# Kernel optimization log

Measured on AMD Instinct MI355X. Metric: run time of the kernel, lower is better.

Reference implementation:

```python
import jax, jax.numpy as jnp
import numpy as np

B, T, C, H = 256, 256, 64, 512


def _uni(key, shape, stdv):
    return jax.random.uniform(key, shape, minval=-stdv, maxval=stdv, dtype=jnp.float32)


def setup_inputs() -> dict:
    key = jax.random.key(0)
    ks = jax.random.split(key, 16)
    data = jax.random.normal(ks[0], (B, T, C), dtype=jnp.float32)
    nan_mask = jax.random.uniform(ks[1], (B, T, C)) < 0.2
    data = jnp.where(nan_mask, jnp.nan, data)
    s_lstm = 1.0 / np.sqrt(H)
    s_c = 1.0 / np.sqrt(C)
    s_h = 1.0 / np.sqrt(H)
    return {
        'data': data,
        # LSTMCell (input = 2*C), PyTorch gate order i,f,g,o
        'W_ih': _uni(ks[2], (4 * H, 2 * C), s_lstm),
        'W_hh': _uni(ks[3], (4 * H, H), s_lstm),
        'b_ih': _uni(ks[4], (4 * H,), s_lstm),
        'b_hh': _uni(ks[5], (4 * H,), s_lstm),
        # temp_decay_h: TemporalDecay(C -> H), stdv = 1/sqrt(W.size(0)) = 1/sqrt(H)
        'W_gh': _uni(ks[6], (H, C), s_h),
        'b_gh': _uni(ks[7], (H,), s_h),
        # temp_decay_x: diag TemporalDecay(C -> C)
        'W_gx': _uni(ks[8], (C, C), s_c),
        'b_gx': _uni(ks[9], (C,), s_c),
        # hist_reg: Linear(H -> C)
        'W_hist': _uni(ks[10], (C, H), s_h),
        'b_hist': _uni(ks[11], (C,), s_h),
        'W_feat': _uni(ks[12], (C, C), s_c),
        'b_feat': _uni(ks[13], (C,), s_c),
        # weight_combine: Linear(2C -> C)
        'W_comb': _uni(ks[14], (C, 2 * C), 1.0 / np.sqrt(2 * C)),
        'b_comb': _uni(ks[15], (C,), 1.0 / np.sqrt(2 * C)),
    }


def delta_calc(masks):
    # masks: [B, T, C]. delta[:,0]=0; delta[:,1]=1; for t>=2:
    # decay = 1 if mask[:,t-1]==1 else decay+1, delta[:,t]=decay.
    b, t, c = masks.shape
    m_prev = jnp.moveaxis(masks[:, 1:t - 1, :], 1, 0)  # [T-2, B, C]

    def step(decay, mp):
        nd = jnp.where(mp == 1.0, 1.0, decay + 1.0)
        return nd, nd

    _, ds = jax.lax.scan(step, jnp.ones((b, c), masks.dtype), m_prev)
    return jnp.concatenate(
        [jnp.zeros((b, 1, c), masks.dtype),
         jnp.ones((b, 1, c), masks.dtype),
         jnp.moveaxis(ds, 0, 1)], axis=1)


def reference(data, W_ih, W_hh, b_ih, b_hh, W_gh, b_gh, W_gx, b_gx,
              W_hist, b_hist, W_feat, b_feat, W_comb, b_comb):
    masks = (~jnp.isnan(data)).astype(data.dtype)
    values = jnp.nan_to_num(data)
    deltas = delta_calc(masks)
    c_dim = data.shape[-1]
    eye = jnp.eye(c_dim, dtype=data.dtype)
    W_gx_m = W_gx * eye            # diag TemporalDecay mask
    W_feat_m = W_feat * (1.0 - eye)

    xs = (jnp.moveaxis(values, 1, 0), jnp.moveaxis(masks, 1, 0),
          jnp.moveaxis(deltas, 1, 0))  # time-major [T,B,C]

    def step(carry, tmd):
        h, c = carry
        x, m, d = tmd
        gamma_h = jnp.exp(-jax.nn.relu(d @ W_gh.T + b_gh))
        gamma_x = jnp.exp(-jax.nn.relu(d @ W_gx_m.T + b_gx))
        h = h * gamma_h
        x_h = h @ W_hist.T + b_hist
        x_c = m * x + (1.0 - m) * x_h
        z_h = x_c @ W_feat_m.T + b_feat
        alpha = jnp.concatenate([gamma_x, m], axis=1) @ W_comb.T + b_comb
        c_h = alpha * z_h + (1.0 - alpha) * x_h
        c_c = m * x + (1.0 - m) * c_h
        inp = jnp.concatenate([c_c, m], axis=1)
        gates = inp @ W_ih.T + b_ih + h @ W_hh.T + b_hh
        gi, gf, gg, go = jnp.split(gates, 4, axis=1)
        c_new = jax.nn.sigmoid(gf) * c + jax.nn.sigmoid(gi) * jnp.tanh(gg)
        h_new = jax.nn.sigmoid(go) * jnp.tanh(c_new)
        return (h_new, c_new), c_c

    hb = data.shape[0]
    hd = W_hh.shape[1]
    init = (jnp.zeros((hb, hd), data.dtype), jnp.zeros((hb, hd), data.dtype))
    _, imps = jax.lax.scan(step, init, xs)
    return jnp.moveaxis(imps, 0, 1)  # [B, T, C]
```

## Files before the change

kernel.cpp:

```cpp
#include <hip/hip_runtime.h>

typedef unsigned short ushort_t;
typedef unsigned int uint_t;
typedef unsigned long long ull_t;
typedef short v8s __attribute__((ext_vector_type(8)));
typedef float v4f __attribute__((ext_vector_type(4)));

__device__ __forceinline__ float b2f(ushort_t u) {
    uint_t x = ((uint_t)u) << 16;
    float f;
    __builtin_memcpy(&f, &x, 4);
    return f;
}
__device__ __forceinline__ ushort_t f2b(float f) {
    uint_t x;
    __builtin_memcpy(&x, &f, 4);
    uint_t r = (x + 0x7FFFu + ((x >> 16) & 1u)) >> 16;
    return (ushort_t)r;
}

__global__ __launch_bounds__(256) void k_setup(
    const float* __restrict__ Wih, const float* __restrict__ Whh,
    const float* __restrict__ Wgh, const float* __restrict__ Whist,
    const float* __restrict__ Wfeat,
    ushort_t* __restrict__ Wih_b, ushort_t* __restrict__ Whh_b,
    ushort_t* __restrict__ Wgh_b, ushort_t* __restrict__ Whist_b,
    ushort_t* __restrict__ Wfeat_b, ull_t* __restrict__ hbufs) {
    int bid = blockIdx.x, tid = threadIdx.x;
    if (bid < 64) {
        ull_t* p = hbufs + (size_t)bid * 4096 + tid;
#pragma unroll
        for (int i = 0; i < 16; ++i) p[i * 256] = 0;
        return;
    }
    bid -= 64;
    const float* src; ushort_t* dst; int n;
    if (bid < 1024)      { src = Wih;   dst = Wih_b;   n = 262144; }
    else if (bid < 5120) { bid -= 1024; src = Whh;   dst = Whh_b;   n = 1048576; }
    else if (bid < 5248) { bid -= 5120; src = Wgh;   dst = Wgh_b;   n = 32768; }
    else if (bid < 5376) { bid -= 5248; src = Whist; dst = Whist_b; n = 32768; }
    else                 { bid -= 5376; src = Wfeat; dst = Wfeat_b; n = 4096; }
    int i = bid * 256 + tid;
    if (i < n) dst[i] = f2b(src[i]);
}

__global__ __launch_bounds__(256) void k_pre(
    const float* __restrict__ data, const float* __restrict__ Wgx,
    const float* __restrict__ bgx,
    ushort_t* __restrict__ values, ushort_t* __restrict__ masks,
    ushort_t* __restrict__ deltas, ushort_t* __restrict__ gammax) {
    __shared__ int lastl[32][9];
    int tid = threadIdx.x;
    int j = tid >> 5, p = tid & 31;
    int pid = blockIdx.x * 32 + p;
    int b = pid >> 6, c = pid & 63;
    float wd = Wgx[c * 64 + c], bg = bgx[c];
    int t0 = j * 32;
    const float* dp = data + (size_t)b * 16384 + c;
    float v[32]; uint_t bits = 0;
#pragma unroll
    for (int s = 0; s < 32; ++s) {
        float x = dp[(t0 + s) * 64];
        bool obs = (x == x);
        v[s] = obs ? x : 0.f;
        bits |= obs ? (1u << s) : 0u;
    }
    uint_t vb = bits;
    if (j == 0) vb &= ~1u;
    int lastloc = 0;
    if (vb) lastloc = t0 + (31 - __clz(vb));
    lastl[p][j] = lastloc;
    __syncthreads();
    int L = 0;
    for (int jj = 0; jj < j; ++jj) L = max(L, lastl[p][jj]);
#pragma unroll
    for (int s = 0; s < 32; ++s) {
        int t = t0 + s;
        float m = ((bits >> s) & 1) ? 1.f : 0.f;
        float d = (t == 0) ? 0.f : (float)(t - L);
        float sg = d * wd + bg;
        float gx = (sg > 0.f) ? __expf(-sg) : 1.f;
        size_t o = (size_t)t * 16384 + pid;
        values[o] = f2b(v[s]); masks[o] = f2b(m);
        deltas[o] = f2b(d);    gammax[o] = f2b(gx);
        if (((bits >> s) & 1) && t >= 1) L = t;
    }
}

__global__ __launch_bounds__(256) void k_alpha(
    const ushort_t* __restrict__ gammax, const ushort_t* __restrict__ masks,
    const float* __restrict__ Wcomb, const float* __restrict__ bcomb,
    ushort_t* __restrict__ alpha) {
    __shared__ __attribute__((aligned(16))) ushort_t wl[64 * 136];
    __shared__ __attribute__((aligned(16))) ushort_t al[16 * 136];
    int tid = threadIdx.x;
    for (int idx = tid; idx < 8192; idx += 256) {
        int r = idx >> 7, kcol = idx & 127;
        wl[r * 136 + kcol] = f2b(Wcomb[idx]);
    }
    int tb0 = blockIdx.x * 16;
    for (int idx = tid; idx < 2048; idx += 256) {
        int r = idx >> 7, kcol = idx & 127;
        al[r * 136 + kcol] = (kcol < 64)
            ? gammax[(size_t)(tb0 + r) * 64 + kcol]
            : masks[(size_t)(tb0 + r) * 64 + (kcol - 64)];
    }
    __syncthreads();
    int i = tid & 63, rg = (tid >> 6) * 4;
    float bc = bcomb[i];
    float acc[4] = {bc, bc, bc, bc};
#pragma unroll
    for (int k8 = 0; k8 < 16; ++k8) {
        v8s w8 = *(const v8s*)(wl + i * 136 + k8 * 8);
#pragma unroll
        for (int rr = 0; rr < 4; ++rr) {
            v8s a8 = *(const v8s*)(al + (rg + rr) * 136 + k8 * 8);
#pragma unroll
            for (int q = 0; q < 8; ++q)
                acc[rr] += b2f((ushort_t)a8[q]) * b2f((ushort_t)w8[q]);
        }
    }
#pragma unroll
    for (int rr = 0; rr < 4; ++rr)
        alpha[(size_t)(tb0 + rg + rr) * 64 + i] = f2b(acc[rr]);
}

__global__ __launch_bounds__(256, 1) void k_run(
    const ushort_t* __restrict__ values, const ushort_t* __restrict__ masks,
    const ushort_t* __restrict__ deltas, const ushort_t* __restrict__ alpha,
    const ushort_t* __restrict__ Wih, const ushort_t* __restrict__ Whh,
    const float* __restrict__ bih, const float* __restrict__ bhh,
    const ushort_t* __restrict__ Wgh, const float* __restrict__ bgh,
    const ushort_t* __restrict__ Whist, const float* __restrict__ bhist,
    const ushort_t* __restrict__ Wfeat, const float* __restrict__ bfeat,
    ushort_t* __restrict__ hbufs, float* __restrict__ out) {
    __shared__ __attribute__((aligned(16))) ushort_t hlds[16 * 520];
    __shared__ __attribute__((aligned(16))) ushort_t inplds[16 * 136];
    __shared__ __attribute__((aligned(16))) ushort_t xclds[16 * 72];
    __shared__ __attribute__((aligned(16))) ushort_t d1b[16 * 72];
    __shared__ __attribute__((aligned(16))) float gl[4 * 16 * 36];
    __shared__ __attribute__((aligned(16))) float gam[16 * 36];

    int tid = threadIdx.x;
    int w = tid >> 6;
    int lane = tid & 63;
    int l15 = lane & 15, quad = lane >> 4;
    int wg = blockIdx.x;
    int rb = wg & 15, cb = wg >> 4;
    int b0 = rb * 16;

    v8s whhF[2][16], wihF[2][4], whisF[16], wfF[2], wghF[2] = {};
    float biasv[2];
#pragma unroll
    for (int nt2 = 0; nt2 < 2; ++nt2) {
        int hc = cb * 32 + nt2 * 16 + l15;
        int rW = w * 512 + hc;
        const ushort_t* whrow = Whh + (size_t)rW * 512;
        const ushort_t* wirow = Wih + (size_t)rW * 128;
#pragma unroll
        for (int kt = 0; kt < 16; ++kt)
            whhF[nt2][kt] = *(const v8s*)(whrow + kt * 32 + quad * 8);
#pragma unroll
        for (int kt = 0; kt < 4; ++kt)
            wihF[nt2][kt] = *(const v8s*)(wirow + kt * 32 + quad * 8);
        biasv[nt2] = bih[rW] + bhh[rW];
    }
    int colC = w * 16 + l15;
    {
        const ushort_t* hrow = Whist + (size_t)colC * 512;
#pragma unroll
        for (int kt = 0; kt < 16; ++kt)
            whisF[kt] = *(const v8s*)(hrow + kt * 32 + quad * 8);
        const ushort_t* frow = Wfeat + colC * 64;
#pragma unroll
        for (int kt = 0; kt < 2; ++kt) {
            int k0 = kt * 32 + quad * 8;
            v8s bb = *(const v8s*)(frow + k0);
#pragma unroll
            for (int j = 0; j < 8; ++j)
                if (k0 + j == colC) bb[j] = 0;
            wfF[kt] = bb;
        }
    }
    float bghv = 0.f;
    if (w < 2) {
        int gcol = cb * 32 + w * 16 + l15;
        const ushort_t* grow = Wgh + gcol * 64;
#pragma unroll
        for (int kt = 0; kt < 2; ++kt)
            wghF[kt] = *(const v8s*)(grow + kt * 32 + quad * 8);
        bghv = bgh[gcol];
    }
    float bhistv = bhist[colC];
    float bfeatv = bfeat[colC];

    int sf_row = tid >> 3, sf_c4 = (tid & 7) * 4;
    float c_reg4[4] = {0.f, 0.f, 0.f, 0.f};

    for (int t = 0; t < 256; ++t) {
        float v4r[4], m4r[4], a4r[4];
#pragma unroll
        for (int r = 0; r < 4; ++r) {
            int row = quad * 4 + r;
            size_t g = (size_t)t * 16384 + (b0 + row) * 64 + colC;
            v4r[r] = b2f(values[g]);
            m4r[r] = b2f(masks[g]);
            a4r[r] = b2f(alpha[g]);
        }
        v8s mreg = {}, dreg = {};
        if (tid < 128) {
            int row = tid >> 3, c8 = (tid & 7) * 8;
            int tn = (t < 255) ? t + 1 : 255;
            mreg = *(const v8s*)(masks + (size_t)t * 16384 + (b0 + row) * 64 + c8);
            dreg = *(const v8s*)(deltas + (size_t)tn * 16384 + (b0 + row) * 64 + c8);
        }

        if (t == 0) {
            v8s z = {0, 0, 0, 0, 0, 0, 0, 0};
            for (int idx = tid; idx < 1040; idx += 256) ((v8s*)hlds)[idx] = z;
        } else {
            const ushort_t* hb = hbufs + (size_t)(t & 7) * 131072;
            const ull_t* hp[8];
            ull_t hv[8];
#pragma unroll
            for (int i = 0; i < 8; ++i) {
                int c = tid + 256 * i;
                int row = c >> 7, c4 = (c & 127) * 4;
                hp[i] = (const ull_t*)(hb + (b0 + row) * 512 + c4);
                hv[i] = __hip_atomic_load(hp[i], __ATOMIC_RELAXED,
                                          __HIP_MEMORY_SCOPE_AGENT);
            }
            int guard = 0;
            while (true) {
                bool any = false;
#pragma unroll
                for (int i = 0; i < 8; ++i) any |= (hv[i] == 0);
                if (!any || ++guard > (1 << 20)) break;
                __builtin_amdgcn_s_sleep(1);
#pragma unroll
                for (int i = 0; i < 8; ++i)
                    if (hv[i] == 0)
                        hv[i] = __hip_atomic_load(hp[i], __ATOMIC_RELAXED,
                                                  __HIP_MEMORY_SCOPE_AGENT);
            }
#pragma unroll
            for (int i = 0; i < 8; ++i) {
                int c = tid + 256 * i;
                int row = c >> 7, c4 = (c & 127) * 4;
                *(ull_t*)(hlds + row * 520 + c4) =
                    hv[i] - 0x0001000100010001ULL;
            }
        }
        if (tid < 128) {
            int row = tid >> 3, c8 = (tid & 7) * 8;
            *(v8s*)(inplds + row * 136 + 64 + c8) = mreg;
            *(v8s*)(d1b + row * 72 + c8) = dreg;
        }
        __syncthreads();

        v4f accx = {0.f, 0.f, 0.f, 0.f};
        v4f accg0 = {0.f, 0.f, 0.f, 0.f}, accg1 = {0.f, 0.f, 0.f, 0.f};
#pragma unroll
        for (int kt = 0; kt < 16; ++kt) {
            v8s a = *(const v8s*)(hlds + l15 * 520 + kt * 32 + quad * 8);
            accx = __builtin_amdgcn_mfma_f32_16x16x32_bf16(a, whisF[kt], accx, 0, 0, 0);
            accg0 = __builtin_amdgcn_mfma_f32_16x16x32_bf16(a, whhF[0][kt], accg0, 0, 0, 0);
            accg1 = __builtin_amdgcn_mfma_f32_16x16x32_bf16(a, whhF[1][kt], accg1, 0, 0, 0);
        }
        if (w < 2) {
            v4f acc = {0.f, 0.f, 0.f, 0.f};
#pragma unroll
            for (int kt = 0; kt < 2; ++kt) {
                v8s a = *(const v8s*)(d1b + l15 * 72 + kt * 32 + quad * 8);
                acc = __builtin_amdgcn_mfma_f32_16x16x32_bf16(a, wghF[kt], acc, 0, 0, 0);
            }
#pragma unroll
            for (int r = 0; r < 4; ++r) {
                float s = acc[r] + bghv;
                gam[(quad * 4 + r) * 36 + w * 16 + l15] = (s > 0.f) ? __expf(-s) : 1.f;
            }
        }
        float xh4[4];
#pragma unroll
        for (int r = 0; r < 4; ++r) {
            float xh = accx[r] + bhistv;
            float xc = m4r[r] * v4r[r] + (1.f - m4r[r]) * xh;
            xclds[(quad * 4 + r) * 72 + colC] = f2b(xc);
            xh4[r] = xh;
        }
        __syncthreads();

        {
            v4f accz = {0.f, 0.f, 0.f, 0.f};
#pragma unroll
            for (int kt = 0; kt < 2; ++kt) {
                v8s a = *(const v8s*)(xclds + l15 * 72 + kt * 32 + quad * 8);
                accz = __builtin_amdgcn_mfma_f32_16x16x32_bf16(a, wfF[kt], accz, 0, 0, 0);
            }
#pragma unroll
            for (int r = 0; r < 4; ++r) {
                float zh = accz[r] + bfeatv;
                float ch = a4r[r] * zh + (1.f - a4r[r]) * xh4[r];
                float cc = m4r[r] * v4r[r] + (1.f - m4r[r]) * ch;
                int row = quad * 4 + r;
                inplds[row * 136 + colC] = f2b(cc);
                if (cb == 0)
                    out[(size_t)(b0 + row) * 16384 + t * 64 + colC] = cc;
            }
        }
        __syncthreads();

#pragma unroll
        for (int nt2 = 0; nt2 < 2; ++nt2) {
            v4f acc = (nt2 == 0) ? accg0 : accg1;
#pragma unroll
            for (int kt = 0; kt < 4; ++kt) {
                v8s a = *(const v8s*)(inplds + l15 * 136 + kt * 32 + quad * 8);
                acc = __builtin_amdgcn_mfma_f32_16x16x32_bf16(a, wihF[nt2][kt], acc, 0, 0, 0);
            }
#pragma unroll
            for (int r = 0; r < 4; ++r)
                gl[w * 576 + (quad * 4 + r) * 36 + nt2 * 16 + l15] = acc[r] + biasv[nt2];
        }
        __syncthreads();

        if (tid < 128) {
            ull_t outv = 0;
#pragma unroll
            for (int j = 0; j < 4; ++j) {
                int hcl = sf_c4 + j;
                float gi = gl[0 * 576 + sf_row * 36 + hcl];
                float gf = gl[1 * 576 + sf_row * 36 + hcl];
                float gg = gl[2 * 576 + sf_row * 36 + hcl];
                float go = gl[3 * 576 + sf_row * 36 + hcl];
                float si = 1.f / (1.f + __expf(-gi));
                float sf = 1.f / (1.f + __expf(-gf));
                float tg = 1.f - 2.f / (__expf(2.f * gg) + 1.f);
                float so = 1.f / (1.f + __expf(-go));
                float cn = sf * c_reg4[j] + si * tg;
                c_reg4[j] = cn;
                float hn = so * (1.f - 2.f / (__expf(2.f * cn) + 1.f));
                float g = gam[sf_row * 36 + hcl];
                outv |= (ull_t)(ushort_t)(f2b(hn * g) + 1) << (16 * j);
            }
            size_t myoff = (size_t)(b0 + sf_row) * 512 + cb * 32 + sf_c4;
            if (t < 255) {
                ushort_t* hnx = hbufs + (size_t)((t + 1) & 7) * 131072;
                __hip_atomic_store((ull_t*)(hnx + myoff), outv,
                                   __ATOMIC_RELAXED, __HIP_MEMORY_SCOPE_AGENT);
            }
            if (t + 4 < 256) {
                ushort_t* hz = hbufs + (size_t)((t + 4) & 7) * 131072;
                __hip_atomic_store((ull_t*)(hz + myoff), 0ULL,
                                   __ATOMIC_RELAXED, __HIP_MEMORY_SCOPE_AGENT);
            }
        }
        __syncthreads();
    }
}

extern "C" void kernel_launch(void* const* d_in, const int* in_sizes, int n_in,
                              void* d_out, int out_size, void* d_ws, size_t ws_size,
                              hipStream_t stream) {
    const float* data  = (const float*)d_in[0];
    const float* Wih   = (const float*)d_in[1];
    const float* Whh   = (const float*)d_in[2];
    const float* bih   = (const float*)d_in[3];
    const float* bhh   = (const float*)d_in[4];
    const float* Wgh   = (const float*)d_in[5];
    const float* bgh   = (const float*)d_in[6];
    const float* Wgx   = (const float*)d_in[7];
    const float* bgx   = (const float*)d_in[8];
    const float* Whist = (const float*)d_in[9];
    const float* bhist = (const float*)d_in[10];
    const float* Wfeat = (const float*)d_in[11];
    const float* bfeat = (const float*)d_in[12];
    const float* Wcomb = (const float*)d_in[13];
    const float* bcomb = (const float*)d_in[14];
    float* out = (float*)d_out;

    char* ws = (char*)d_ws;
    const size_t NTBC = 256UL * 256 * 64;
    ushort_t* valuesb = (ushort_t*)ws; ws += NTBC * 2;
    ushort_t* masksp  = (ushort_t*)ws; ws += NTBC * 2;
    ushort_t* deltasp = (ushort_t*)ws; ws += NTBC * 2;
    ushort_t* gammax  = (ushort_t*)ws; ws += NTBC * 2;
    ushort_t* alphap  = (ushort_t*)ws; ws += NTBC * 2;
    ushort_t* Wih_b   = (ushort_t*)ws; ws += 2048UL * 128 * 2;
    ushort_t* Whh_b   = (ushort_t*)ws; ws += 2048UL * 512 * 2;
    ushort_t* Wgh_b   = (ushort_t*)ws; ws += 512UL * 64 * 2;
    ushort_t* Whist_b = (ushort_t*)ws; ws += 64UL * 512 * 2;
    ushort_t* Wfeat_b = (ushort_t*)ws; ws += 64UL * 64 * 2;
    ushort_t* hbufs   = (ushort_t*)ws; ws += 8UL * 131072 * 2;

    k_setup<<<5456, 256, 0, stream>>>(Wih, Whh, Wgh, Whist, Wfeat,
                                      Wih_b, Whh_b, Wgh_b, Whist_b, Wfeat_b,
                                      (ull_t*)hbufs);
    k_pre<<<512, 256, 0, stream>>>(data, Wgx, bgx, valuesb, masksp, deltasp, gammax);
    k_alpha<<<4096, 256, 0, stream>>>(gammax, masksp, Wcomb, bcomb, alphap);
    k_run<<<256, 256, 0, stream>>>(valuesb, masksp, deltasp, alphap,
                                   Wih_b, Whh_b, bih, bhh,
                                   Wgh_b, bgh, Whist_b, bhist,
                                   Wfeat_b, bfeat, hbufs, out);
}
```

Baseline: 973.0 us.

## Prefetch next-step inputs, use MFMA in alpha kernel, lighter barriers, spread output writes

The recurrent kernel now loads the per-step values, masks, alpha and deltas for the next timestep while the current step runs, which takes global load latency off the serial path. Its __syncthreads calls become a custom barrier that waits only on LDS counters. Gate and gamma LDS rows are padded to 44 floats so they can be read as vectors, and poll addresses are computed once. Output writes rotate across column-blocks instead of always coming from cb==0. The alpha kernel is rewritten around bf16 MFMA with 64 rows per block. Risks are higher register pressure and relying on correct ordering with a weaker barrier.

```diff
diff --git a/kernel.cpp b/kernel.cpp
--- a/kernel.cpp
+++ b/kernel.cpp
@@ -17,6 +17,12 @@
     __builtin_memcpy(&x, &f, 4);
     uint_t r = (x + 0x7FFFu + ((x >> 16) & 1u)) >> 16;
     return (ushort_t)r;
+}
+
+__device__ __forceinline__ void wg_bar() {
+    asm volatile("s_waitcnt lgkmcnt(0)" ::: "memory");
+    __builtin_amdgcn_s_barrier();
+    asm volatile("" ::: "memory");
 }
 
 __global__ __launch_bounds__(256) void k_setup(
@@ -92,37 +98,41 @@
     const float* __restrict__ Wcomb, const float* __restrict__ bcomb,
     ushort_t* __restrict__ alpha) {
     __shared__ __attribute__((aligned(16))) ushort_t wl[64 * 136];
-    __shared__ __attribute__((aligned(16))) ushort_t al[16 * 136];
+    __shared__ __attribute__((aligned(16))) ushort_t al[64 * 136];
     int tid = threadIdx.x;
     for (int idx = tid; idx < 8192; idx += 256) {
         int r = idx >> 7, kcol = idx & 127;
         wl[r * 136 + kcol] = f2b(Wcomb[idx]);
     }
-    int tb0 = blockIdx.x * 16;
-    for (int idx = tid; idx < 2048; idx += 256) {
+    int tb0 = blockIdx.x * 64;
+    for (int idx = tid; idx < 8192; idx += 256) {
         int r = idx >> 7, kcol = idx & 127;
         al[r * 136 + kcol] = (kcol < 64)
             ? gammax[(size_t)(tb0 + r) * 64 + kcol]
             : masks[(size_t)(tb0 + r) * 64 + (kcol - 64)];
     }
     __syncthreads();
-    int i = tid & 63, rg = (tid >> 6) * 4;
-    float bc = bcomb[i];
-    float acc[4] = {bc, bc, bc, bc};
-#pragma unroll
-    for (int k8 = 0; k8 < 16; ++k8) {
-        v8s w8 = *(const v8s*)(wl + i * 136 + k8 * 8);
-#pragma unroll
-        for (int rr = 0; rr < 4; ++rr) {
-            v8s a8 = *(const v8s*)(al + (rg + rr) * 136 + k8 * 8);
-#pragma unroll
-            for (int q = 0; q < 8; ++q)
-                acc[rr] += b2f((ushort_t)a8[q]) * b2f((ushort_t)w8[q]);
-        }
-    }
-#pragma unroll
-    for (int rr = 0; rr < 4; ++rr)
-        alpha[(size_t)(tb0 + rg + rr) * 64 + i] = f2b(acc[rr]);
+    int w = tid >> 6, lane = tid & 63, l15 = lane & 15, quad = lane >> 4;
+    v4f acc[4] = {};
+#pragma unroll
+    for (int kt = 0; kt < 4; ++kt) {
+        v8s a = *(const v8s*)(al + (w * 16 + l15) * 136 + kt * 32 + quad * 8);
+#pragma unroll
+        for (int nt = 0; nt < 4; ++nt) {
+            v8s bfr = *(const v8s*)(wl + (nt * 16 + l15) * 136 + kt * 32 + quad * 8);
+            acc[nt] = __builtin_amdgcn_mfma_f32_16x16x32_bf16(a, bfr, acc[nt], 0, 0, 0);
+        }
+    }
+#pragma unroll
+    for (int nt = 0; nt < 4; ++nt) {
+        int col = nt * 16 + l15;
+        float bc = bcomb[col];
+#pragma unroll
+        for (int j = 0; j < 4; ++j) {
+            int row = w * 16 + quad * 4 + j;
+            alpha[(size_t)(tb0 + row) * 64 + col] = f2b(acc[nt][j] + bc);
+        }
+    }
 }
 
 __global__ __launch_bounds__(256, 1) void k_run(
@@ -138,8 +148,8 @@
     __shared__ __attribute__((aligned(16))) ushort_t inplds[16 * 136];
     __shared__ __attribute__((aligned(16))) ushort_t xclds[16 * 72];
     __shared__ __attribute__((aligned(16))) ushort_t d1b[16 * 72];
-    __shared__ __attribute__((aligned(16))) float gl[4 * 16 * 36];
-    __shared__ __attribute__((aligned(16))) float gam[16 * 36];
+    __shared__ __attribute__((aligned(16))) float gl[4 * 16 * 44];
+    __shared__ __attribute__((aligned(16))) float gam[16 * 44];
 
     int tid = threadIdx.x;
     int w = tid >> 6;
@@ -195,41 +205,46 @@
     float bfeatv = bfeat[colC];
 
     int sf_row = tid >> 3, sf_c4 = (tid & 7) * 4;
+    int srow = sf_row, sc8 = (tid & 7) * 8;
+
+    int pollQ[8], ldsB[8];
+#pragma unroll
+    for (int i = 0; i < 8; ++i) {
+        int c = tid + 256 * i;
+        int row = c >> 7, c4 = (c & 127) * 4;
+        pollQ[i] = ((b0 + row) * 512 + c4) >> 2;
+        ldsB[i] = row * 520 + c4;
+    }
+
+    ushort_t vraw[4], mraw[4], araw[4];
+    v8s mregc = {}, dregc = {};
+#pragma unroll
+    for (int r = 0; r < 4; ++r) {
+        size_t g = (size_t)(b0 + quad * 4 + r) * 64 + colC;
+        vraw[r] = values[g]; mraw[r] = masks[g]; araw[r] = alpha[g];
+    }
+    if (tid < 128) {
+        mregc = *(const v8s*)(masks + (size_t)(b0 + srow) * 64 + sc8);
+        dregc = *(const v8s*)(deltas + 16384 + (size_t)(b0 + srow) * 64 + sc8);
+    }
+
     float c_reg4[4] = {0.f, 0.f, 0.f, 0.f};
 
     for (int t = 0; t < 256; ++t) {
-        float v4r[4], m4r[4], a4r[4];
-#pragma unroll
-        for (int r = 0; r < 4; ++r) {
-            int row = quad * 4 + r;
-            size_t g = (size_t)t * 16384 + (b0 + row) * 64 + colC;
-            v4r[r] = b2f(values[g]);
-            m4r[r] = b2f(masks[g]);
-            a4r[r] = b2f(alpha[g]);
-        }
-        v8s mreg = {}, dreg = {};
         if (tid < 128) {
-            int row = tid >> 3, c8 = (tid & 7) * 8;
-            int tn = (t < 255) ? t + 1 : 255;
-            mreg = *(const v8s*)(masks + (size_t)t * 16384 + (b0 + row) * 64 + c8);
-            dreg = *(const v8s*)(deltas + (size_t)tn * 16384 + (b0 + row) * 64 + c8);
-        }
-
+            *(v8s*)(inplds + srow * 136 + 64 + sc8) = mregc;
+            *(v8s*)(d1b + srow * 72 + sc8) = dregc;
+        }
         if (t == 0) {
             v8s z = {0, 0, 0, 0, 0, 0, 0, 0};
             for (int idx = tid; idx < 1040; idx += 256) ((v8s*)hlds)[idx] = z;
         } else {
-            const ushort_t* hb = hbufs + (size_t)(t & 7) * 131072;
-            const ull_t* hp[8];
+            const ull_t* hq = (const ull_t*)(hbufs + (size_t)(t & 7) * 131072);
             ull_t hv[8];
 #pragma unroll
-            for (int i = 0; i < 8; ++i) {
-                int c = tid + 256 * i;
-                int row = c >> 7, c4 = (c & 127) * 4;
-                hp[i] = (const ull_t*)(hb + (b0 + row) * 512 + c4);
-                hv[i] = __hip_atomic_load(hp[i], __ATOMIC_RELAXED,
+            for (int i = 0; i < 8; ++i)
+                hv[i] = __hip_atomic_load(hq + pollQ[i], __ATOMIC_RELAXED,
                                           __HIP_MEMORY_SCOPE_AGENT);
-            }
             int guard = 0;
             while (true) {
                 bool any = false;
@@ -240,23 +255,31 @@
 #pragma unroll
                 for (int i = 0; i < 8; ++i)
                     if (hv[i] == 0)
-                        hv[i] = __hip_atomic_load(hp[i], __ATOMIC_RELAXED,
+                        hv[i] = __hip_atomic_load(hq + pollQ[i], __ATOMIC_RELAXED,
                                                   __HIP_MEMORY_SCOPE_AGENT);
             }
 #pragma unroll
-            for (int i = 0; i < 8; ++i) {
-                int c = tid + 256 * i;
-                int row = c >> 7, c4 = (c & 127) * 4;
-                *(ull_t*)(hlds + row * 520 + c4) =
-                    hv[i] - 0x0001000100010001ULL;
-            }
-        }
-        if (tid < 128) {
-            int row = tid >> 3, c8 = (tid & 7) * 8;
-            *(v8s*)(inplds + row * 136 + 64 + c8) = mreg;
-            *(v8s*)(d1b + row * 72 + c8) = dreg;
-        }
-        __syncthreads();
+            for (int i = 0; i < 8; ++i)
+                *(ull_t*)(hlds + ldsB[i]) = hv[i] - 0x0001000100010001ULL;
+        }
+        ushort_t vnx[4], mnx[4], anx[4];
+        v8s mregn = mregc, dregn = dregc;
+        {
+            int tp = (t < 255) ? t + 1 : 255;
+            int tq = (t < 254) ? t + 2 : 255;
+            size_t gb = (size_t)tp * 16384;
+#pragma unroll
+            for (int r = 0; r < 4; ++r) {
+                size_t g = gb + (size_t)(b0 + quad * 4 + r) * 64 + colC;
+                vnx[r] = values[g]; mnx[r] = masks[g]; anx[r] = alpha[g];
+            }
+            if (tid < 128) {
+                mregn = *(const v8s*)(masks + gb + (size_t)(b0 + srow) * 64 + sc8);
+                dregn = *(const v8s*)(deltas + (size_t)tq * 16384 +
+                                      (size_t)(b0 + srow) * 64 + sc8);
+            }
+        }
+        wg_bar();
 
         v4f accx = {0.f, 0.f, 0.f, 0.f};
         v4f accg0 = {0.f, 0.f, 0.f, 0.f}, accg1 = {0.f, 0.f, 0.f, 0.f};
@@ -277,10 +300,14 @@
 #pragma unroll
             for (int r = 0; r < 4; ++r) {
                 float s = acc[r] + bghv;
-                gam[(quad * 4 + r) * 36 + w * 16 + l15] = (s > 0.f) ? __expf(-s) : 1.f;
-            }
-        }
-        float xh4[4];
+                gam[(quad * 4 + r) * 44 + w * 16 + l15] = (s > 0.f) ? __expf(-s) : 1.f;
+            }
+        }
+        float v4r[4], m4r[4], a4r[4], xh4[4];
+#pragma unroll
+        for (int r = 0; r < 4; ++r) {
+            v4r[r] = b2f(vraw[r]); m4r[r] = b2f(mraw[r]); a4r[r] = b2f(araw[r]);
+        }
 #pragma unroll
         for (int r = 0; r < 4; ++r) {
             float xh = accx[r] + bhistv;
@@ -288,7 +315,7 @@
             xclds[(quad * 4 + r) * 72 + colC] = f2b(xc);
             xh4[r] = xh;
         }
-        __syncthreads();
+        wg_bar();
 
         {
             v4f accz = {0.f, 0.f, 0.f, 0.f};
@@ -297,6 +324,7 @@
                 v8s a = *(const v8s*)(xclds + l15 * 72 + kt * 32 + quad * 8);
                 accz = __builtin_amdgcn_mfma_f32_16x16x32_bf16(a, wfF[kt], accz, 0, 0, 0);
             }
+            bool wout = (cb == (t & 15));
 #pragma unroll
             for (int r = 0; r < 4; ++r) {
                 float zh = accz[r] + bfeatv;
@@ -304,11 +332,11 @@
                 float cc = m4r[r] * v4r[r] + (1.f - m4r[r]) * ch;
                 int row = quad * 4 + r;
                 inplds[row * 136 + colC] = f2b(cc);
-                if (cb == 0)
+                if (wout)
                     out[(size_t)(b0 + row) * 16384 + t * 64 + colC] = cc;
             }
         }
-        __syncthreads();
+        wg_bar();
 
 #pragma unroll
         for (int nt2 = 0; nt2 < 2; ++nt2) {
@@ -320,19 +348,20 @@
             }
 #pragma unroll
             for (int r = 0; r < 4; ++r)
-                gl[w * 576 + (quad * 4 + r) * 36 + nt2 * 16 + l15] = acc[r] + biasv[nt2];
-        }
-        __syncthreads();
+                gl[w * 704 + (quad * 4 + r) * 44 + nt2 * 16 + l15] = acc[r] + biasv[nt2];
+        }
+        wg_bar();
 
         if (tid < 128) {
+            v4f g0 = *(const v4f*)(gl + 0 * 704 + sf_row * 44 + sf_c4);
+            v4f g1 = *(const v4f*)(gl + 1 * 704 + sf_row * 44 + sf_c4);
+            v4f g2 = *(const v4f*)(gl + 2 * 704 + sf_row * 44 + sf_c4);
+            v4f g3 = *(const v4f*)(gl + 3 * 704 + sf_row * 44 + sf_c4);
+            v4f gm = *(const v4f*)(gam + sf_row * 44 + sf_c4);
             ull_t outv = 0;
 #pragma unroll
             for (int j = 0; j < 4; ++j) {
-                int hcl = sf_c4 + j;
-                float gi = gl[0 * 576 + sf_row * 36 + hcl];
-                float gf = gl[1 * 576 + sf_row * 36 + hcl];
-                float gg = gl[2 * 576 + sf_row * 36 + hcl];
-                float go = gl[3 * 576 + sf_row * 36 + hcl];
+                float gi = g0[j], gf = g1[j], gg = g2[j], go = g3[j];
                 float si = 1.f / (1.f + __expf(-gi));
                 float sf = 1.f / (1.f + __expf(-gf));
                 float tg = 1.f - 2.f / (__expf(2.f * gg) + 1.f);
@@ -340,8 +369,7 @@
                 float cn = sf * c_reg4[j] + si * tg;
                 c_reg4[j] = cn;
                 float hn = so * (1.f - 2.f / (__expf(2.f * cn) + 1.f));
-                float g = gam[sf_row * 36 + hcl];
-                outv |= (ull_t)(ushort_t)(f2b(hn * g) + 1) << (16 * j);
+                outv |= (ull_t)(ushort_t)(f2b(hn * gm[j]) + 1) << (16 * j);
             }
             size_t myoff = (size_t)(b0 + sf_row) * 512 + cb * 32 + sf_c4;
             if (t < 255) {
@@ -355,7 +383,13 @@
                                    __ATOMIC_RELAXED, __HIP_MEMORY_SCOPE_AGENT);
             }
         }
-        __syncthreads();
+        wg_bar();
+
+#pragma unroll
+        for (int r = 0; r < 4; ++r) {
+            vraw[r] = vnx[r]; mraw[r] = mnx[r]; araw[r] = anx[r];
+        }
+        mregc = mregn; dregc = dregn;
     }
 }
 
@@ -397,7 +431,7 @@
                                       Wih_b, Whh_b, Wgh_b, Whist_b, Wfeat_b,
                                       (ull_t*)hbufs);
     k_pre<<<512, 256, 0, stream>>>(data, Wgx, bgx, valuesb, masksp, deltasp, gammax);
-    k_alpha<<<4096, 256, 0, stream>>>(gammax, masksp, Wcomb, bcomb, alphap);
+    k_alpha<<<1024, 256, 0, stream>>>(gammax, masksp, Wcomb, bcomb, alphap);
     k_run<<<256, 256, 0, stream>>>(valuesb, masksp, deltasp, alphap,
                                    Wih_b, Whh_b, bih, bhh,
                                    Wgh_b, bgh, Whist_b, bhist,
```

New measurement: 1.123 ms. 1.15x slower.
